# Optimization experiments

Hardware: AMD Instinct MI355X
Metric: run time of the kernel (lower is better)

The kernel has to match this reference:

```python
import jax, jax.numpy as jnp
import numpy as np

BN_EPS = 1e-5
NUM_HEADS = 16


def setup_inputs() -> dict:
    key = jax.random.key(0)
    k1, k2 = jax.random.split(key)
    B, F, E = 8, 1024, 1024
    x = jax.random.normal(k1, (B, F, E), dtype=jnp.float32)
    # xavier_uniform for Linear(E, 3E): bound = sqrt(6/(E + 3E))
    bound = float(np.sqrt(6.0 / (E + 3 * E)))
    W_qkv = jax.random.uniform(k2, (3 * E, E), minval=-bound, maxval=bound, dtype=jnp.float32)
    b_qkv = jnp.zeros((3 * E,), dtype=jnp.float32)
    gamma = jnp.ones((F,), dtype=jnp.float32)
    beta = jnp.zeros((F,), dtype=jnp.float32)
    return {"x": x, "gamma": gamma, "beta": beta, "W_qkv": W_qkv, "b_qkv": b_qkv}


def reference(x, gamma, beta, W_qkv, b_qkv):
    B, F, E = x.shape
    H = NUM_HEADS
    hd = E // H
    # BatchNorm1d(features_dim) in training mode: channels = F axis,
    # stats over (batch, embed) dims, biased variance.
    mean = jnp.mean(x, axis=(0, 2), keepdims=True)          # [1,F,1]
    var = jnp.mean((x - mean) ** 2, axis=(0, 2), keepdims=True)
    xn = (x - mean) * jax.lax.rsqrt(var + BN_EPS)
    xn = xn * gamma[None, :, None] + beta[None, :, None]
    # QKV projection: torch Linear -> xn @ W^T + b
    qkv = jnp.einsum('bfe,oe->bfo', xn, W_qkv) + b_qkv       # [B,F,3E]
    qkv = qkv.reshape(B, F, H, 3 * hd).transpose(0, 2, 1, 3) # [B,H,F,3hd]
    q, k, v = jnp.split(qkv, 3, axis=-1)                     # each [B,H,F,hd]
    scale = 1.0 / jnp.sqrt(jnp.float32(hd))
    logits = jnp.einsum('bhqd,bhkd->bhqk', q, k) * scale     # [B,H,F,F]
    attn = jax.nn.softmax(logits, axis=-1)
    values = jnp.einsum('bhqk,bhkd->bhqd', attn, v)          # [B,H,F,hd]
    values = values.transpose(0, 2, 1, 3).reshape(B, F, E)
    return values
```

## Files before the change

### kernel.cpp

```cpp
#include <hip/hip_runtime.h>

typedef unsigned short u16;
typedef unsigned int   u32;

typedef __bf16 bf16x8 __attribute__((ext_vector_type(8)));
typedef float  f32x4  __attribute__((ext_vector_type(4)));

typedef const __attribute__((address_space(1))) void* gas_ptr;
typedef __attribute__((address_space(3))) void* las_ptr;

__device__ __forceinline__ u16 f2bf(float f) {
  u32 u = __builtin_bit_cast(u32, f);
  u += 0x7fffu + ((u >> 16) & 1u);
  return (u16)(u >> 16);
}
__device__ __forceinline__ float bf2f(u16 u) {
  return __builtin_bit_cast(float, ((u32)u) << 16);
}
__device__ __forceinline__ u32 cvtpk(float a, float b) {
  u32 r;
  asm("v_cvt_pk_bf16_f32 %0, %1, %2" : "=v"(r) : "v"(a), "v"(b));
  return r;
}

__global__ __launch_bounds__(256) void bn_norm_kernel(
    const float* __restrict__ x, const float* __restrict__ gamma,
    const float* __restrict__ beta, u16* __restrict__ xn) {
  const int F = 1024, E = 1024;
  int f = blockIdx.x;
  __shared__ float sh[8192];
  __shared__ float ps[4], pq[4], sc[2];

  const float* xf = x + (size_t)f * E;
  float ls = 0.f, lq = 0.f;
  for (int i = threadIdx.x; i < 8192; i += 256) {
    int b = i >> 10, e = i & 1023;
    float v = xf[(size_t)b * F * E + e];
    sh[i] = v;
    ls += v;
    lq += v * v;
  }
  #pragma unroll
  for (int o = 32; o > 0; o >>= 1) {
    ls += __shfl_down(ls, o, 64);
    lq += __shfl_down(lq, o, 64);
  }
  int w = threadIdx.x >> 6;
  if ((threadIdx.x & 63) == 0) { ps[w] = ls; pq[w] = lq; }
  __syncthreads();
  if (threadIdx.x == 0) {
    float s = ps[0] + ps[1] + ps[2] + ps[3];
    float q = pq[0] + pq[1] + pq[2] + pq[3];
    float mean = s * (1.f / 8192.f);
    float var = q * (1.f / 8192.f) - mean * mean;
    float scale = gamma[f] * rsqrtf(var + 1e-5f);
    sc[0] = scale;
    sc[1] = beta[f] - mean * scale;
  }
  __syncthreads();
  float scale = sc[0], shift = sc[1];
  for (int i = threadIdx.x; i < 8192; i += 256) {
    int b = i >> 10, e = i & 1023;
    xn[((size_t)(b * F + f)) * E + e] = f2bf(sh[i] * scale + shift);
  }
}

__global__ __launch_bounds__(256) void wconv_kernel(
    const float* __restrict__ W, u16* __restrict__ Wb) {
  const int total = 3072 * 1024 / 4;
  for (int i = blockIdx.x * 256 + threadIdx.x; i < total; i += gridDim.x * 256) {
    float4 v = ((const float4*)W)[i];
    ushort4 o;
    o.x = f2bf(v.x); o.y = f2bf(v.y); o.z = f2bf(v.z); o.w = f2bf(v.w);
    ((ushort4*)Wb)[i] = o;
  }
}

__global__ __launch_bounds__(256) void gemm_qkv_kernel(
    const u16* __restrict__ A, const u16* __restrict__ Bw,
    const float* __restrict__ bias, u16* __restrict__ C) {
  const int K = 1024, N = 3072;
  __shared__ u16 As[128 * 32];
  __shared__ u16 Bs[128 * 32];

  int m0 = blockIdx.x * 128, n0 = blockIdx.y * 128;
  int t = threadIdx.x, lane = t & 63, w = t >> 6;
  int wr = w >> 1, wc = w & 1;
  int r = lane & 15, g = lane >> 4;

  int srow = t >> 2, scol = (t & 3) * 8;
  const u16* gA  = A  + (size_t)(m0 + srow) * K + scol;
  const u16* gA2 = gA + (size_t)64 * K;
  const u16* gB  = Bw + (size_t)(n0 + srow) * K + scol;
  const u16* gB2 = gB + (size_t)64 * K;
  u16* lA  = As + t * 8;
  u16* lA2 = As + 2048 + t * 8;
  u16* lB  = Bs + t * 8;
  u16* lB2 = Bs + 2048 + t * 8;

  f32x4 acc[4][4] = {};

  const u16* pA = As + (size_t)(wr * 64 + r) * 32 + g * 8;
  const u16* pB = Bs + (size_t)(wc * 64 + r) * 32 + g * 8;

  for (int k0 = 0; k0 < K; k0 += 32) {
    __builtin_amdgcn_global_load_lds((gas_ptr)gA,  (las_ptr)lA,  16, 0, 0);
    __builtin_amdgcn_global_load_lds((gas_ptr)gA2, (las_ptr)lA2, 16, 0, 0);
    __builtin_amdgcn_global_load_lds((gas_ptr)gB,  (las_ptr)lB,  16, 0, 0);
    __builtin_amdgcn_global_load_lds((gas_ptr)gB2, (las_ptr)lB2, 16, 0, 0);
    gA += 32; gA2 += 32; gB += 32; gB2 += 32;
    __syncthreads();

    bf16x8 af[4], bfr[4];
    #pragma unroll
    for (int mi = 0; mi < 4; ++mi)
      af[mi] = __builtin_bit_cast(bf16x8, *(const int4*)(pA + mi * 512));
    #pragma unroll
    for (int ni = 0; ni < 4; ++ni)
      bfr[ni] = __builtin_bit_cast(bf16x8, *(const int4*)(pB + ni * 512));
    #pragma unroll
    for (int mi = 0; mi < 4; ++mi)
      #pragma unroll
      for (int ni = 0; ni < 4; ++ni)
        acc[mi][ni] = __builtin_amdgcn_mfma_f32_16x16x32_bf16(af[mi], bfr[ni], acc[mi][ni], 0, 0, 0);
    __syncthreads();
  }

  #pragma unroll
  for (int ni = 0; ni < 4; ++ni) {
    int col = n0 + wc * 64 + ni * 16 + r;
    float bv = bias[col];
    #pragma unroll
    for (int mi = 0; mi < 4; ++mi) {
      int row = m0 + wr * 64 + mi * 16 + g * 4;
      #pragma unroll
      for (int j = 0; j < 4; ++j)
        C[(size_t)(row + j) * N + col] = f2bf(acc[mi][ni][j] + bv);
    }
  }
}

__global__ __launch_bounds__(256) void vt_kernel(
    const u16* __restrict__ qkv, u16* __restrict__ Vt) {
  __shared__ u16 T[64][72];
  int bh = blockIdx.y, b = bh >> 4, h = bh & 15;
  int f0 = blockIdx.x * 64;
  int t = threadIdx.x;
  int fl = t >> 2, c16 = (t & 3) * 16;
  const u16* src = qkv + (size_t)(b * 1024 + f0 + fl) * 3072 + h * 192 + 128 + c16;
  *(int4*)&T[fl][c16]     = *(const int4*)src;
  *(int4*)&T[fl][c16 + 8] = *(const int4*)(src + 8);
  __syncthreads();
  int dl = t >> 2, fc = (t & 3) * 16;
  u16 buf[16];
  #pragma unroll
  for (int j = 0; j < 16; ++j) {
    int c = fc + j;
    int m = c & 31;
    int a = ((m & 4) << 2) | ((m & 16) >> 1) | ((m & 8) >> 1) | (m & 3);
    buf[j] = T[(c & 32) | a][dl];
  }
  u16* dst = Vt + (size_t)bh * 65536 + (size_t)dl * 1024 + f0 + fc;
  *(int4*)dst       = *(int4*)&buf[0];
  *(int4*)(dst + 8) = *(int4*)&buf[8];
}

__global__ __launch_bounds__(256) void attn_kernel(
    const u16* __restrict__ qkv, const u16* __restrict__ Vt,
    float* __restrict__ out) {
  const int F = 1024, NQ = 3072;
  int bid = blockIdx.x;
  int xcd = bid & 7;
  int li  = bid >> 3;
  int bh  = ((li >> 4) << 3) | xcd;
  int ql  = li & 15;
  int w   = threadIdx.x >> 6;
  int lane = threadIdx.x & 63;
  int q = lane & 15, g = lane >> 4;
  int qs = q & 7;
  int q0 = ql * 64 + w * 16;
  int b = bh >> 4, h = bh & 15;

  const u16* base = qkv + (size_t)b * F * NQ + h * 192;
  const u16* VtBH = Vt + (size_t)bh * 65536;

  __shared__ u16 S[16384];

  int i8 = lane >> 3;
  int ic = lane & 7;

  const float qscale = 0.125f * 1.4426950408889634f;
  bf16x8 Qf0, Qf1;
  {
    const u16* qp = base + (size_t)(q0 + q) * NQ + g * 8;
    union { int4 v; u16 u[8]; } uu0, uu1;
    uu0.v = *(const int4*)(qp);
    uu1.v = *(const int4*)(qp + 32);
    union { u32 w4[4]; bf16x8 v; } p0, p1;
    #pragma unroll
    for (int j = 0; j < 4; ++j) {
      p0.w4[j] = cvtpk(bf2f(uu0.u[2 * j]) * qscale, bf2f(uu0.u[2 * j + 1]) * qscale);
      p1.w4[j] = cvtpk(bf2f(uu1.u[2 * j]) * qscale, bf2f(uu1.u[2 * j + 1]) * qscale);
    }
    Qf0 = p0.v; Qf1 = p1.v;
  }

  f32x4 acc[4] = {};
  float m = 0.0f, lsum = 0.f;

  #define STAGE(buf, kt)                                                       \
    do {                                                                       \
      int kb_ = (kt) * 64;                                                     \
      _Pragma("unroll")                                                        \
      for (int rr = 0; rr < 2; ++rr) {                                         \
        int r_ = rr * 32 + w * 8 + i8;                                         \
        int sc_ = (ic ^ (r_ & 7)) * 8;                                         \
        const u16* ks_ = base + (size_t)(kb_ + r_) * NQ + 64 + sc_;            \
        const u16* vs_ = VtBH + (size_t)r_ * 1024 + kb_ + sc_;                 \
        __builtin_amdgcn_global_load_lds((gas_ptr)ks_,                         \
            (las_ptr)&S[(buf) * 4096 + (rr * 32 + w * 8) * 64], 16, 0, 0);     \
        __builtin_amdgcn_global_load_lds((gas_ptr)vs_,                         \
            (las_ptr)&S[8192 + (buf) * 4096 + (rr * 32 + w * 8) * 64], 16, 0, 0);\
      }                                                                        \
    } while (0)

  STAGE(0, 0);
  __syncthreads();

  int cur = 0;
  for (int kt = 0; kt < 16; ++kt) {
    if (kt < 15) STAGE(cur ^ 1, kt + 1);

    const u16* Kb = &S[cur * 4096];
    const u16* Vb = &S[8192 + cur * 4096];

    f32x4 s[4];
    f32x4 seed = {-m, -m, -m, -m};
    __builtin_amdgcn_s_setprio(1);
    #pragma unroll
    for (int ks = 0; ks < 4; ++ks) {
      int row = ks * 16 + q;
      int4 k0 = *(const int4*)&Kb[row * 64 + ((g ^ qs) * 8)];
      int4 k1 = *(const int4*)&Kb[row * 64 + (((4 + g) ^ qs) * 8)];
      f32x4 sv = seed;
      sv = __builtin_amdgcn_mfma_f32_16x16x32_bf16(__builtin_bit_cast(bf16x8, k0), Qf0, sv, 0, 0, 0);
      sv = __builtin_amdgcn_mfma_f32_16x16x32_bf16(__builtin_bit_cast(bf16x8, k1), Qf1, sv, 0, 0, 0);
      s[ks] = sv;
    }
    __builtin_amdgcn_s_setprio(0);

    float a0 = fmaxf(fmaxf(s[0][0], s[0][1]), s[0][2]);
    float a1 = fmaxf(fmaxf(s[0][3], s[1][0]), s[1][1]);
    float a2 = fmaxf(fmaxf(s[1][2], s[1][3]), s[2][0]);
    float a3 = fmaxf(fmaxf(s[2][1], s[2][2]), s[2][3]);
    float a4 = fmaxf(fmaxf(s[3][0], s[3][1]), s[3][2]);
    float tmx = fmaxf(fmaxf(fmaxf(a0, a1), a2), fmaxf(fmaxf(a3, a4), s[3][3]));

    float p[16];
    if (__builtin_expect(__any(tmx > 8.0f), 0)) {
      float tr = fmaxf(tmx, __shfl_xor(tmx, 16, 64));
      tr = fmaxf(tr, __shfl_xor(tr, 32, 64));
      float dm = fmaxf(tr, 0.f);
      float alpha = exp2f(-dm);
      lsum *= alpha;
      acc[0] *= alpha; acc[1] *= alpha; acc[2] *= alpha; acc[3] *= alpha;
      m += dm;
      #pragma unroll
      for (int ks = 0; ks < 4; ++ks) {
        p[ks * 4 + 0] = exp2f(s[ks][0] - dm);
        p[ks * 4 + 1] = exp2f(s[ks][1] - dm);
        p[ks * 4 + 2] = exp2f(s[ks][2] - dm);
        p[ks * 4 + 3] = exp2f(s[ks][3] - dm);
      }
    } else {
      #pragma unroll
      for (int ks = 0; ks < 4; ++ks) {
        p[ks * 4 + 0] = exp2f(s[ks][0]);
        p[ks * 4 + 1] = exp2f(s[ks][1]);
        p[ks * 4 + 2] = exp2f(s[ks][2]);
        p[ks * 4 + 3] = exp2f(s[ks][3]);
      }
    }
    float q01 = p[0] + p[1],   q23 = p[2] + p[3];
    float q45 = p[4] + p[5],   q67 = p[6] + p[7];
    float q89 = p[8] + p[9],   qab = p[10] + p[11];
    float qcd = p[12] + p[13], qef = p[14] + p[15];
    lsum += ((q01 + q23) + (q45 + q67)) + ((q89 + qab) + (qcd + qef));

    union { u32 w4[4]; bf16x8 v; } pb0, pb1;
    pb0.w4[0] = cvtpk(p[0], p[1]);   pb0.w4[1] = cvtpk(p[2], p[3]);
    pb0.w4[2] = cvtpk(p[4], p[5]);   pb0.w4[3] = cvtpk(p[6], p[7]);
    pb1.w4[0] = cvtpk(p[8], p[9]);   pb1.w4[1] = cvtpk(p[10], p[11]);
    pb1.w4[2] = cvtpk(p[12], p[13]); pb1.w4[3] = cvtpk(p[14], p[15]);

    __builtin_amdgcn_s_setprio(1);
    #pragma unroll
    for (int dt = 0; dt < 4; ++dt) {
      int row = dt * 16 + q;
      int4 v0 = *(const int4*)&Vb[row * 64 + ((g ^ qs) * 8)];
      int4 v1 = *(const int4*)&Vb[row * 64 + (((4 + g) ^ qs) * 8)];
      acc[dt] = __builtin_amdgcn_mfma_f32_16x16x32_bf16(__builtin_bit_cast(bf16x8, v0), pb0.v, acc[dt], 0, 0, 0);
      acc[dt] = __builtin_amdgcn_mfma_f32_16x16x32_bf16(__builtin_bit_cast(bf16x8, v1), pb1.v, acc[dt], 0, 0, 0);
    }
    __builtin_amdgcn_s_setprio(0);

    __syncthreads();
    cur ^= 1;
  }
  #undef STAGE

  lsum += __shfl_xor(lsum, 16, 64);
  lsum += __shfl_xor(lsum, 32, 64);
  float inv = 1.0f / lsum;

  float* oT = (float*)S + (size_t)w * 1088;
  #pragma unroll
  for (int dt = 0; dt < 4; ++dt) {
    oT[(dt * 16 + g * 4 + 0) * 17 + q] = acc[dt][0] * inv;
    oT[(dt * 16 + g * 4 + 1) * 17 + q] = acc[dt][1] * inv;
    oT[(dt * 16 + g * 4 + 2) * 17 + q] = acc[dt][2] * inv;
    oT[(dt * 16 + g * 4 + 3) * 17 + q] = acc[dt][3] * inv;
  }
  asm volatile("s_waitcnt lgkmcnt(0)" ::: "memory");
  int oq = lane >> 2, dc = (lane & 3) * 16;
  float* orow = out + (size_t)(b * F + q0 + oq) * 1024 + h * 64 + dc;
  #pragma unroll
  for (int c4 = 0; c4 < 4; ++c4) {
    float4 v;
    v.x = oT[(dc + c4 * 4 + 0) * 17 + oq];
    v.y = oT[(dc + c4 * 4 + 1) * 17 + oq];
    v.z = oT[(dc + c4 * 4 + 2) * 17 + oq];
    v.w = oT[(dc + c4 * 4 + 3) * 17 + oq];
    *(float4*)(orow + c4 * 4) = v;
  }
}

extern "C" void kernel_launch(void* const* d_in, const int* in_sizes, int n_in,
                              void* d_out, int out_size, void* d_ws, size_t ws_size,
                              hipStream_t stream) {
  const float* x     = (const float*)d_in[0];
  const float* gamma = (const float*)d_in[1];
  const float* beta  = (const float*)d_in[2];
  const float* W     = (const float*)d_in[3];
  const float* bias  = (const float*)d_in[4];
  float* out = (float*)d_out;

  char* ws = (char*)d_ws;
  u16* xn  = (u16*)ws;
  u16* Wb  = (u16*)(ws + (size_t)16 * 1024 * 1024);
  u16* qkv = (u16*)(ws + (size_t)22 * 1024 * 1024);
  u16* Vt  = (u16*)(ws + (size_t)70 * 1024 * 1024);

  bn_norm_kernel<<<1024, 256, 0, stream>>>(x, gamma, beta, xn);
  wconv_kernel<<<768, 256, 0, stream>>>(W, Wb);
  gemm_qkv_kernel<<<dim3(64, 24), 256, 0, stream>>>(xn, Wb, bias, qkv);
  vt_kernel<<<dim3(16, 128), 256, 0, stream>>>(qkv, Vt);
  attn_kernel<<<2048, 256, 0, stream>>>(qkv, Vt, out);
}
```

Measured before the change: 167.7 us.

## Process two 16-row query tiles per wave to reuse K/V LDS loads

Each wave now handles 32 query rows as two independent 16-row tiles that share the same K and V fragments read from LDS. This halves the block count and the total global staging of K/V, and halves the LDS reads per MFMA. In exchange register pressure roughly doubles for accumulators and scores, which may lower occupancy, and there are fewer blocks to spread across CUs.

```diff
diff --git a/kernel.cpp b/kernel.cpp
--- a/kernel.cpp
+++ b/kernel.cpp
@@ -172,13 +172,13 @@
   int bid = blockIdx.x;
   int xcd = bid & 7;
   int li  = bid >> 3;
-  int bh  = ((li >> 4) << 3) | xcd;
-  int ql  = li & 15;
+  int bh  = ((li >> 3) << 3) | xcd;
+  int ql  = li & 7;
   int w   = threadIdx.x >> 6;
   int lane = threadIdx.x & 63;
   int q = lane & 15, g = lane >> 4;
   int qs = q & 7;
-  int q0 = ql * 64 + w * 16;
+  int q0 = ql * 128 + w * 32;
   int b = bh >> 4, h = bh & 15;
 
   const u16* base = qkv + (size_t)b * F * NQ + h * 192;
@@ -190,23 +190,28 @@
   int ic = lane & 7;
 
   const float qscale = 0.125f * 1.4426950408889634f;
-  bf16x8 Qf0, Qf1;
+  bf16x8 QfA0, QfA1, QfB0, QfB1;
   {
-    const u16* qp = base + (size_t)(q0 + q) * NQ + g * 8;
-    union { int4 v; u16 u[8]; } uu0, uu1;
-    uu0.v = *(const int4*)(qp);
-    uu1.v = *(const int4*)(qp + 32);
-    union { u32 w4[4]; bf16x8 v; } p0, p1;
+    const u16* qpA = base + (size_t)(q0 + q) * NQ + g * 8;
+    const u16* qpB = qpA + (size_t)16 * NQ;
+    union { int4 v; u16 u[8]; } a0, a1, b0, b1;
+    a0.v = *(const int4*)(qpA);
+    a1.v = *(const int4*)(qpA + 32);
+    b0.v = *(const int4*)(qpB);
+    b1.v = *(const int4*)(qpB + 32);
+    union { u32 w4[4]; bf16x8 v; } pa0, pa1, pb0_, pb1_;
     #pragma unroll
     for (int j = 0; j < 4; ++j) {
-      p0.w4[j] = cvtpk(bf2f(uu0.u[2 * j]) * qscale, bf2f(uu0.u[2 * j + 1]) * qscale);
-      p1.w4[j] = cvtpk(bf2f(uu1.u[2 * j]) * qscale, bf2f(uu1.u[2 * j + 1]) * qscale);
+      pa0.w4[j]  = cvtpk(bf2f(a0.u[2 * j]) * qscale, bf2f(a0.u[2 * j + 1]) * qscale);
+      pa1.w4[j]  = cvtpk(bf2f(a1.u[2 * j]) * qscale, bf2f(a1.u[2 * j + 1]) * qscale);
+      pb0_.w4[j] = cvtpk(bf2f(b0.u[2 * j]) * qscale, bf2f(b0.u[2 * j + 1]) * qscale);
+      pb1_.w4[j] = cvtpk(bf2f(b1.u[2 * j]) * qscale, bf2f(b1.u[2 * j + 1]) * qscale);
     }
-    Qf0 = p0.v; Qf1 = p1.v;
-  }
-
-  f32x4 acc[4] = {};
-  float m = 0.0f, lsum = 0.f;
+    QfA0 = pa0.v; QfA1 = pa1.v; QfB0 = pb0_.v; QfB1 = pb1_.v;
+  }
+
+  f32x4 accA[4] = {}, accB[4] = {};
+  float mA = 0.0f, lsA = 0.f, mB = 0.0f, lsB = 0.f;
 
   #define STAGE(buf, kt)                                                       \
     do {                                                                       \
@@ -224,6 +229,46 @@
       }                                                                        \
     } while (0)
 
+  #define SOFTMAX(s, m_, ls_, acc_, p)                                         \
+    do {                                                                       \
+      float a0_ = fmaxf(fmaxf(s[0][0], s[0][1]), s[0][2]);                     \
+      float a1_ = fmaxf(fmaxf(s[0][3], s[1][0]), s[1][1]);                     \
+      float a2_ = fmaxf(fmaxf(s[1][2], s[1][3]), s[2][0]);                     \
+      float a3_ = fmaxf(fmaxf(s[2][1], s[2][2]), s[2][3]);                     \
+      float a4_ = fmaxf(fmaxf(s[3][0], s[3][1]), s[3][2]);                     \
+      float tmx_ = fmaxf(fmaxf(fmaxf(a0_, a1_), a2_),                          \
+                         fmaxf(fmaxf(a3_, a4_), s[3][3]));                     \
+      if (__builtin_expect(__any(tmx_ > 8.0f), 0)) {                           \
+        float tr_ = fmaxf(tmx_, __shfl_xor(tmx_, 16, 64));                     \
+        tr_ = fmaxf(tr_, __shfl_xor(tr_, 32, 64));                             \
+        float dm_ = fmaxf(tr_, 0.f);                                           \
+        float al_ = exp2f(-dm_);                                               \
+        ls_ *= al_;                                                            \
+        acc_[0] *= al_; acc_[1] *= al_; acc_[2] *= al_; acc_[3] *= al_;        \
+        m_ += dm_;                                                             \
+        _Pragma("unroll")                                                      \
+        for (int ks_ = 0; ks_ < 4; ++ks_) {                                    \
+          p[ks_ * 4 + 0] = exp2f(s[ks_][0] - dm_);                             \
+          p[ks_ * 4 + 1] = exp2f(s[ks_][1] - dm_);                             \
+          p[ks_ * 4 + 2] = exp2f(s[ks_][2] - dm_);                             \
+          p[ks_ * 4 + 3] = exp2f(s[ks_][3] - dm_);                             \
+        }                                                                      \
+      } else {                                                                 \
+        _Pragma("unroll")                                                      \
+        for (int ks_ = 0; ks_ < 4; ++ks_) {                                    \
+          p[ks_ * 4 + 0] = exp2f(s[ks_][0]);                                   \
+          p[ks_ * 4 + 1] = exp2f(s[ks_][1]);                                   \
+          p[ks_ * 4 + 2] = exp2f(s[ks_][2]);                                   \
+          p[ks_ * 4 + 3] = exp2f(s[ks_][3]);                                   \
+        }                                                                      \
+      }                                                                        \
+      float q01_ = p[0] + p[1],   q23_ = p[2] + p[3];                          \
+      float q45_ = p[4] + p[5],   q67_ = p[6] + p[7];                          \
+      float q89_ = p[8] + p[9],   qab_ = p[10] + p[11];                        \
+      float qcd_ = p[12] + p[13], qef_ = p[14] + p[15];                        \
+      ls_ += ((q01_ + q23_) + (q45_ + q67_)) + ((q89_ + qab_) + (qcd_ + qef_));\
+    } while (0)
+
   STAGE(0, 0);
   __syncthreads();
 
@@ -234,64 +279,39 @@
     const u16* Kb = &S[cur * 4096];
     const u16* Vb = &S[8192 + cur * 4096];
 
-    f32x4 s[4];
-    f32x4 seed = {-m, -m, -m, -m};
+    f32x4 sA[4], sB[4];
+    f32x4 seedA = {-mA, -mA, -mA, -mA};
+    f32x4 seedB = {-mB, -mB, -mB, -mB};
     __builtin_amdgcn_s_setprio(1);
     #pragma unroll
     for (int ks = 0; ks < 4; ++ks) {
       int row = ks * 16 + q;
       int4 k0 = *(const int4*)&Kb[row * 64 + ((g ^ qs) * 8)];
       int4 k1 = *(const int4*)&Kb[row * 64 + (((4 + g) ^ qs) * 8)];
-      f32x4 sv = seed;
-      sv = __builtin_amdgcn_mfma_f32_16x16x32_bf16(__builtin_bit_cast(bf16x8, k0), Qf0, sv, 0, 0, 0);
-      sv = __builtin_amdgcn_mfma_f32_16x16x32_bf16(__builtin_bit_cast(bf16x8, k1), Qf1, sv, 0, 0, 0);
-      s[ks] = sv;
+      f32x4 va = seedA;
+      va = __builtin_amdgcn_mfma_f32_16x16x32_bf16(__builtin_bit_cast(bf16x8, k0), QfA0, va, 0, 0, 0);
+      va = __builtin_amdgcn_mfma_f32_16x16x32_bf16(__builtin_bit_cast(bf16x8, k1), QfA1, va, 0, 0, 0);
+      sA[ks] = va;
+      f32x4 vb = seedB;
+      vb = __builtin_amdgcn_mfma_f32_16x16x32_bf16(__builtin_bit_cast(bf16x8, k0), QfB0, vb, 0, 0, 0);
+      vb = __builtin_amdgcn_mfma_f32_16x16x32_bf16(__builtin_bit_cast(bf16x8, k1), QfB1, vb, 0, 0, 0);
+      sB[ks] = vb;
     }
     __builtin_amdgcn_s_setprio(0);
 
-    float a0 = fmaxf(fmaxf(s[0][0], s[0][1]), s[0][2]);
-    float a1 = fmaxf(fmaxf(s[0][3], s[1][0]), s[1][1]);
-    float a2 = fmaxf(fmaxf(s[1][2], s[1][3]), s[2][0]);
-    float a3 = fmaxf(fmaxf(s[2][1], s[2][2]), s[2][3]);
-    float a4 = fmaxf(fmaxf(s[3][0], s[3][1]), s[3][2]);
-    float tmx = fmaxf(fmaxf(fmaxf(a0, a1), a2), fmaxf(fmaxf(a3, a4), s[3][3]));
-
-    float p[16];
-    if (__builtin_expect(__any(tmx > 8.0f), 0)) {
-      float tr = fmaxf(tmx, __shfl_xor(tmx, 16, 64));
-      tr = fmaxf(tr, __shfl_xor(tr, 32, 64));
-      float dm = fmaxf(tr, 0.f);
-      float alpha = exp2f(-dm);
-      lsum *= alpha;
-      acc[0] *= alpha; acc[1] *= alpha; acc[2] *= alpha; acc[3] *= alpha;
-      m += dm;
-      #pragma unroll
-      for (int ks = 0; ks < 4; ++ks) {
-        p[ks * 4 + 0] = exp2f(s[ks][0] - dm);
-        p[ks * 4 + 1] = exp2f(s[ks][1] - dm);
-        p[ks * 4 + 2] = exp2f(s[ks][2] - dm);
-        p[ks * 4 + 3] = exp2f(s[ks][3] - dm);
-      }
-    } else {
-      #pragma unroll
-      for (int ks = 0; ks < 4; ++ks) {
-        p[ks * 4 + 0] = exp2f(s[ks][0]);
-        p[ks * 4 + 1] = exp2f(s[ks][1]);
-        p[ks * 4 + 2] = exp2f(s[ks][2]);
-        p[ks * 4 + 3] = exp2f(s[ks][3]);
-      }
-    }
-    float q01 = p[0] + p[1],   q23 = p[2] + p[3];
-    float q45 = p[4] + p[5],   q67 = p[6] + p[7];
-    float q89 = p[8] + p[9],   qab = p[10] + p[11];
-    float qcd = p[12] + p[13], qef = p[14] + p[15];
-    lsum += ((q01 + q23) + (q45 + q67)) + ((q89 + qab) + (qcd + qef));
-
-    union { u32 w4[4]; bf16x8 v; } pb0, pb1;
-    pb0.w4[0] = cvtpk(p[0], p[1]);   pb0.w4[1] = cvtpk(p[2], p[3]);
-    pb0.w4[2] = cvtpk(p[4], p[5]);   pb0.w4[3] = cvtpk(p[6], p[7]);
-    pb1.w4[0] = cvtpk(p[8], p[9]);   pb1.w4[1] = cvtpk(p[10], p[11]);
-    pb1.w4[2] = cvtpk(p[12], p[13]); pb1.w4[3] = cvtpk(p[14], p[15]);
+    float pA[16], pB[16];
+    SOFTMAX(sA, mA, lsA, accA, pA);
+    SOFTMAX(sB, mB, lsB, accB, pB);
+
+    union { u32 w4[4]; bf16x8 v; } pbA0, pbA1, pbB0, pbB1;
+    pbA0.w4[0] = cvtpk(pA[0], pA[1]);   pbA0.w4[1] = cvtpk(pA[2], pA[3]);
+    pbA0.w4[2] = cvtpk(pA[4], pA[5]);   pbA0.w4[3] = cvtpk(pA[6], pA[7]);
+    pbA1.w4[0] = cvtpk(pA[8], pA[9]);   pbA1.w4[1] = cvtpk(pA[10], pA[11]);
+    pbA1.w4[2] = cvtpk(pA[12], pA[13]); pbA1.w4[3] = cvtpk(pA[14], pA[15]);
+    pbB0.w4[0] = cvtpk(pB[0], pB[1]);   pbB0.w4[1] = cvtpk(pB[2], pB[3]);
+    pbB0.w4[2] = cvtpk(pB[4], pB[5]);   pbB0.w4[3] = cvtpk(pB[6], pB[7]);
+    pbB1.w4[0] = cvtpk(pB[8], pB[9]);   pbB1.w4[1] = cvtpk(pB[10], pB[11]);
+    pbB1.w4[2] = cvtpk(pB[12], pB[13]); pbB1.w4[3] = cvtpk(pB[14], pB[15]);
 
     __builtin_amdgcn_s_setprio(1);
     #pragma unroll
@@ -299,8 +319,10 @@
       int row = dt * 16 + q;
       int4 v0 = *(const int4*)&Vb[row * 64 + ((g ^ qs) * 8)];
       int4 v1 = *(const int4*)&Vb[row * 64 + (((4 + g) ^ qs) * 8)];
-      acc[dt] = __builtin_amdgcn_mfma_f32_16x16x32_bf16(__builtin_bit_cast(bf16x8, v0), pb0.v, acc[dt], 0, 0, 0);
-      acc[dt] = __builtin_amdgcn_mfma_f32_16x16x32_bf16(__builtin_bit_cast(bf16x8, v1), pb1.v, acc[dt], 0, 0, 0);
+      accA[dt] = __builtin_amdgcn_mfma_f32_16x16x32_bf16(__builtin_bit_cast(bf16x8, v0), pbA0.v, accA[dt], 0, 0, 0);
+      accA[dt] = __builtin_amdgcn_mfma_f32_16x16x32_bf16(__builtin_bit_cast(bf16x8, v1), pbA1.v, accA[dt], 0, 0, 0);
+      accB[dt] = __builtin_amdgcn_mfma_f32_16x16x32_bf16(__builtin_bit_cast(bf16x8, v0), pbB0.v, accB[dt], 0, 0, 0);
+      accB[dt] = __builtin_amdgcn_mfma_f32_16x16x32_bf16(__builtin_bit_cast(bf16x8, v1), pbB1.v, accB[dt], 0, 0, 0);
     }
     __builtin_amdgcn_s_setprio(0);
 
@@ -308,31 +330,41 @@
     cur ^= 1;
   }
   #undef STAGE
-
-  lsum += __shfl_xor(lsum, 16, 64);
-  lsum += __shfl_xor(lsum, 32, 64);
-  float inv = 1.0f / lsum;
+  #undef SOFTMAX
 
   float* oT = (float*)S + (size_t)w * 1088;
-  #pragma unroll
-  for (int dt = 0; dt < 4; ++dt) {
-    oT[(dt * 16 + g * 4 + 0) * 17 + q] = acc[dt][0] * inv;
-    oT[(dt * 16 + g * 4 + 1) * 17 + q] = acc[dt][1] * inv;
-    oT[(dt * 16 + g * 4 + 2) * 17 + q] = acc[dt][2] * inv;
-    oT[(dt * 16 + g * 4 + 3) * 17 + q] = acc[dt][3] * inv;
-  }
-  asm volatile("s_waitcnt lgkmcnt(0)" ::: "memory");
   int oq = lane >> 2, dc = (lane & 3) * 16;
-  float* orow = out + (size_t)(b * F + q0 + oq) * 1024 + h * 64 + dc;
-  #pragma unroll
-  for (int c4 = 0; c4 < 4; ++c4) {
-    float4 v;
-    v.x = oT[(dc + c4 * 4 + 0) * 17 + oq];
-    v.y = oT[(dc + c4 * 4 + 1) * 17 + oq];
-    v.z = oT[(dc + c4 * 4 + 2) * 17 + oq];
-    v.w = oT[(dc + c4 * 4 + 3) * 17 + oq];
-    *(float4*)(orow + c4 * 4) = v;
-  }
+
+  #define EPILOGUE(acc_, ls_, qbase)                                           \
+    do {                                                                       \
+      float l_ = ls_;                                                          \
+      l_ += __shfl_xor(l_, 16, 64);                                            \
+      l_ += __shfl_xor(l_, 32, 64);                                            \
+      float inv_ = 1.0f / l_;                                                  \
+      _Pragma("unroll")                                                        \
+      for (int dt = 0; dt < 4; ++dt) {                                         \
+        oT[(dt * 16 + g * 4 + 0) * 17 + q] = acc_[dt][0] * inv_;               \
+        oT[(dt * 16 + g * 4 + 1) * 17 + q] = acc_[dt][1] * inv_;               \
+        oT[(dt * 16 + g * 4 + 2) * 17 + q] = acc_[dt][2] * inv_;               \
+        oT[(dt * 16 + g * 4 + 3) * 17 + q] = acc_[dt][3] * inv_;               \
+      }                                                                        \
+      asm volatile("s_waitcnt lgkmcnt(0)" ::: "memory");                       \
+      float* orow_ = out + (size_t)(b * F + (qbase) + oq) * 1024 + h * 64 + dc;\
+      _Pragma("unroll")                                                        \
+      for (int c4 = 0; c4 < 4; ++c4) {                                         \
+        float4 v_;                                                             \
+        v_.x = oT[(dc + c4 * 4 + 0) * 17 + oq];                                \
+        v_.y = oT[(dc + c4 * 4 + 1) * 17 + oq];                                \
+        v_.z = oT[(dc + c4 * 4 + 2) * 17 + oq];                                \
+        v_.w = oT[(dc + c4 * 4 + 3) * 17 + oq];                                \
+        *(float4*)(orow_ + c4 * 4) = v_;                                       \
+      }                                                                        \
+      asm volatile("s_waitcnt lgkmcnt(0)" ::: "memory");                       \
+    } while (0)
+
+  EPILOGUE(accA, lsA, q0);
+  EPILOGUE(accB, lsB, q0 + 16);
+  #undef EPILOGUE
 }
 
 extern "C" void kernel_launch(void* const* d_in, const int* in_sizes, int n_in,
@@ -355,5 +387,5 @@
   wconv_kernel<<<768, 256, 0, stream>>>(W, Wb);
   gemm_qkv_kernel<<<dim3(64, 24), 256, 0, stream>>>(xn, Wb, bias, qkv);
   vt_kernel<<<dim3(16, 128), 256, 0, stream>>>(qkv, Vt);
-  attn_kernel<<<2048, 256, 0, stream>>>(qkv, Vt, out);
-}
+  attn_kernel<<<1024, 256, 0, stream>>>(qkv, Vt, out);
+}
```

Measured after the change: 170.4 us. About the same (+1.6%).
